# Kernel optimization log

Hardware: AMD Instinct MI355X
Metric: run time of the kernel (lower is better)

Reference implementation:

```python
import jax, jax.numpy as jnp
import numpy as np

B, H_IMG, W_IMG, DIM, HEADS, WS = 8, 56, 56, 768, 12, 14
SEQ = H_IMG * W_IMG
HEAD_DIM = DIM // HEADS
MLP_HID = 4 * DIM
SCALE = HEAD_DIM ** -0.5


def setup_inputs() -> dict:
    key = jax.random.key(0)
    ks = jax.random.split(key, 8)
    s = 0.02
    return {
        "x": jax.random.normal(ks[0], (B, SEQ, DIM), jnp.float32),
        "ln1_scale": jnp.ones((DIM,), jnp.float32),
        "ln1_bias": jnp.zeros((DIM,), jnp.float32),
        "qkv_w": jax.random.normal(ks[1], (DIM, 3 * DIM), jnp.float32) * s,
        "qkv_b": jnp.zeros((3 * DIM,), jnp.float32),
        "rel_pos_h": jax.random.normal(ks[2], (2 * WS - 1, HEAD_DIM), jnp.float32) * s,
        "rel_pos_w": jax.random.normal(ks[3], (2 * WS - 1, HEAD_DIM), jnp.float32) * s,
        "proj_w": jax.random.normal(ks[4], (DIM, DIM), jnp.float32) * s,
        "proj_b": jnp.zeros((DIM,), jnp.float32),
        "ln2_scale": jnp.ones((DIM,), jnp.float32),
        "ln2_bias": jnp.zeros((DIM,), jnp.float32),
        "fc1_w": jax.random.normal(ks[5], (DIM, MLP_HID), jnp.float32) * s,
        "fc1_b": jnp.zeros((MLP_HID,), jnp.float32),
        "fc2_w": jax.random.normal(ks[6], (MLP_HID, DIM), jnp.float32) * s,
        "fc2_b": jnp.zeros((DIM,), jnp.float32),
        "H": H_IMG,
        "W": W_IMG,
    }


def _layernorm(x, scale, bias, eps=1e-5):
    mu = x.mean(-1, keepdims=True)
    var = x.var(-1, keepdims=True)
    return (x - mu) / jnp.sqrt(var + eps) * scale + bias


def _window_attn(x, H, W, qkv_w, qkv_b, rel_pos_h, rel_pos_w, proj_w, proj_b):
    # x: (B, H*W, C); H, W divisible by WS so the torch pad branch is a no-op
    Bn, N, C = x.shape
    nh, nw = H // WS, W // WS
    # window_partition: (B, H, W, C) -> (B*nh*nw, WS*WS, C)
    xw = (x.reshape(Bn, nh, WS, nw, WS, C)
            .transpose(0, 1, 3, 2, 4, 5)
            .reshape(-1, WS * WS, C))
    Bw, Nw = xw.shape[0], WS * WS
    qkv = (xw @ qkv_w + qkv_b).reshape(Bw, Nw, 3, HEADS, HEAD_DIM).transpose(2, 0, 3, 1, 4)
    q = qkv[0] * SCALE  # scaled q also used for rel-pos terms (matches torch)
    k, v = qkv[1], qkv[2]
    attn = jnp.einsum('bhnd,bhmd->bhnm', q, k)  # (Bw, heads, Nw, Nw)
    # relative position bias (q_shape == k_shape == (WS, WS), ratios == 1)
    dist = jnp.arange(WS)[:, None] - jnp.arange(WS)[None, :] + (WS - 1)
    Rh = rel_pos_h[dist]  # (WS, WS, head_dim)
    Rw = rel_pos_w[dist]
    r_q = q.reshape(Bw, HEADS, WS, WS, HEAD_DIM)
    rel_h = jnp.einsum('byhwc,hkc->byhwk', r_q, Rh)
    rel_w = jnp.einsum('byhwc,wkc->byhwk', r_q, Rw)
    attn = (attn.reshape(Bw, HEADS, WS, WS, WS, WS)
            + rel_h[:, :, :, :, :, None]
            + rel_w[:, :, :, :, None, :]).reshape(Bw, HEADS, Nw, Nw)
    attn = jax.nn.softmax(attn, axis=-1)
    out = jnp.einsum('bhnm,bhmd->bhnd', attn, v).transpose(0, 2, 1, 3).reshape(Bw, Nw, C)
    out = out @ proj_w + proj_b
    # window_reverse: (Bw, WS*WS, C) -> (B, H*W, C)
    out = (out.reshape(Bn, nh, nw, WS, WS, C)
              .transpose(0, 1, 3, 2, 4, 5)
              .reshape(Bn, H * W, C))
    return out


def reference(x, ln1_scale, ln1_bias, qkv_w, qkv_b, rel_pos_h, rel_pos_w,
              proj_w, proj_b, ln2_scale, ln2_bias, fc1_w, fc1_b, fc2_w, fc2_b, H, W):
    a = _window_attn(_layernorm(x, ln1_scale, ln1_bias), H, W,
                     qkv_w, qkv_b, rel_pos_h, rel_pos_w, proj_w, proj_b)
    x = x + a
    h = _layernorm(x, ln2_scale, ln2_bias)
    h = jax.nn.gelu(h @ fc1_w + fc1_b, approximate=False)  # torch nn.GELU is exact erf
    x = x + (h @ fc2_w + fc2_b)
    return x
```

## Files before the change

kernel.cpp:

```cpp
#include <hip/hip_runtime.h>
#include <stdint.h>

typedef unsigned short u16;
typedef __bf16 bf16x8 __attribute__((ext_vector_type(8)));
typedef float f32x4 __attribute__((ext_vector_type(4)));
typedef unsigned uint32x4 __attribute__((ext_vector_type(4)));

#define DEVI __device__ __forceinline__

static constexpr int DIM = 768;
static constexpr int SEQL = 3136;
static constexpr int MROWS = 25088;
static constexpr int HEADS = 12;
static constexpr int HD = 64;
static constexpr int NW = 196;
static constexpr float QSCALE = 0.125f;
static constexpr int ATTN_SMEM = 72704;
static constexpr int GEMM_SMEM = 49152;

DEVI float b2f(u16 u) { union { unsigned i; float f; } v; v.i = ((unsigned)u) << 16; return v.f; }
DEVI u16 f2b(float f) { union { float f; unsigned u; } v; v.f = f; return (u16)((v.u + 0x7FFFu + ((v.u >> 16) & 1u)) >> 16); }
DEVI unsigned pack2(float a, float b) { return (unsigned)f2b(a) | ((unsigned)f2b(b) << 16); }
DEVI bf16x8 u4bf(uint4 u) { union { uint4 a; bf16x8 b; } c; c.a = u; return c.b; }

DEVI void gl_lds16(const void* g, void* l) {
  __builtin_amdgcn_global_load_lds((const __attribute__((address_space(1))) void*)g,
                                   (__attribute__((address_space(3))) void*)l, 16, 0, 0);
}

DEVI bf16x8 ldg_b8(const u16* p) {
  union { uint4 u; bf16x8 v; } r;
  const uint2* p2 = (const uint2*)p;
  uint2 lo = p2[0], hi = p2[1];
  r.u.x = lo.x; r.u.y = lo.y; r.u.z = hi.x; r.u.w = hi.y;
  return r.v;
}

__global__ __launch_bounds__(256) void pack_b(const float* __restrict__ in,
                                              u16* __restrict__ out, int K, int N) {
  int f8 = blockIdx.x * 256 + threadIdx.x;
  int l = f8 & 63;
  int rest = f8 >> 6;
  int s = rest & 1, nf = (rest >> 1) & 3, wn2 = (rest >> 3) & 1, kt = rest >> 4;
  int bn = blockIdx.y;
  int n = bn * 128 + wn2 * 64 + nf * 16 + (l & 15);
  int kb = kt * 64 + s * 32 + (l >> 4) * 8;
  size_t obase = (((size_t)bn * (K >> 6) + kt) * 2 + wn2) * 4096 + (nf * 2 + s) * 512 + (size_t)l * 8;
  #pragma unroll
  for (int e = 0; e < 8; ++e)
    out[obase + e] = f2b(in[(size_t)(kb + e) * N + n]);
}

__global__ __launch_bounds__(256) void cvt_rpb(const float* __restrict__ rph,
                                               const float* __restrict__ rpw,
                                               u16* __restrict__ rpb) {
  int i = blockIdx.x * 256 + threadIdx.x;
  int tbl = i >> 11, r = (i >> 6) & 31, c = i & 63;
  float v = (r < 27) ? (tbl ? rpw : rph)[r * 64 + c] : 0.f;
  rpb[i] = f2b(v);
}

template<bool REMAP>
__global__ __launch_bounds__(256) void ln_kernel(const float* __restrict__ xin,
                                                 const float* __restrict__ g,
                                                 const float* __restrict__ bb,
                                                 u16* __restrict__ outw) {
  __shared__ float red[8];
  const int r = blockIdx.x;
  const int tid = threadIdx.x;
  const float* xr = xin + (size_t)r * DIM;
  float v0 = xr[tid], v1 = xr[tid + 256], v2 = xr[tid + 512];
  float s1 = v0 + v1 + v2;
  float s2 = v0 * v0 + v1 * v1 + v2 * v2;
  #pragma unroll
  for (int o = 32; o > 0; o >>= 1) { s1 += __shfl_down(s1, o); s2 += __shfl_down(s2, o); }
  const int l = tid & 63, w = tid >> 6;
  if (l == 0) { red[w] = s1; red[w + 4] = s2; }
  __syncthreads();
  float ts = red[0] + red[1] + red[2] + red[3];
  float tss = red[4] + red[5] + red[6] + red[7];
  float mean = ts * (1.f / 768.f);
  float var = tss * (1.f / 768.f) - mean * mean;
  float rstd = rsqrtf(var + 1e-5f);
  size_t orow;
  if constexpr (REMAP) {
    int b = r / SEQL, s = r % SEQL;
    int h = s / 56, ww = s % 56;
    orow = (size_t)(b * 16 + (h / 14) * 4 + (ww / 14)) * NW + (h % 14) * 14 + (ww % 14);
  } else {
    orow = (size_t)r;
  }
  u16* orp = outw + orow * DIM;
  orp[tid]       = f2b((v0 - mean) * rstd * g[tid]       + bb[tid]);
  orp[tid + 256] = f2b((v1 - mean) * rstd * g[tid + 256] + bb[tid + 256]);
  orp[tid + 512] = f2b((v2 - mean) * rstd * g[tid + 512] + bb[tid + 512]);
}

struct Epi {
  const float* bias;
  const float* x;
  float* outf;
  u16* q; u16* k; u16* v;
  u16* o16;
};

#define MFMA_BF16 __builtin_amdgcn_mfma_f32_16x16x32_bf16

template<int K, int N, int EPI>
__global__ __launch_bounds__(256, 3)
void gemm6_ep(const u16* __restrict__ A, const u16* __restrict__ Bp, Epi ep) {
  extern __shared__ __align__(16) char gsm[];

  constexpr int NBN = N / 128;
  constexpr int NSTC = NBN / 6;
  constexpr int NKT = K / 64;

  const int tid = threadIdx.x;
  const int l = tid & 63, w = tid >> 6;
  const int lr = l & 15, lg = l >> 4;

  const int nwg = gridDim.x;
  const int cpx = nwg >> 3;
  const int wg = (blockIdx.x & 7) * cpx + (blockIdx.x >> 3);
  const int st = wg / 42, r42 = wg - st * 42;
  const int bm = (st / NSTC) * 7 + r42 / 6;
  const int bn = (st - (st / NSTC) * NSTC) * 6 + r42 - (r42 / 6) * 6;
  const int wm = (w >> 1) * 64, wn = (w & 1) * 64;

  const u16* Ab = A + (size_t)bm * 128 * K;
  const u16* Bw = Bp + (((size_t)bn * NKT) * 2 + (w & 1)) * 4096 + (size_t)l * 8;

  int srcoff[4];
  #pragma unroll
  for (int p = 0; p < 4; ++p) {
    int si = p * 256 + tid;
    int row = si >> 3;
    srcoff[p] = row * K + (((si & 7) ^ (row & 7)) << 3);
  }
  #define STG(kt, buf) do {                                                     \
    char* _d = gsm + (buf) * 16384;                                             \
    _Pragma("unroll")                                                           \
    for (int _p = 0; _p < 4; ++_p)                                              \
      gl_lds16(Ab + srcoff[_p] + (size_t)(kt) * 64, _d + _p * 4096 + tid * 16); \
  } while (0)

  const int p0 = lg ^ (lr & 7);
  const int p1 = p0 ^ 4;

  f32x4 zero4 = {0.f, 0.f, 0.f, 0.f};
  f32x4 acc[4][4];
  #pragma unroll
  for (int i = 0; i < 4; ++i)
    #pragma unroll
    for (int j = 0; j < 4; ++j) acc[i][j] = zero4;

  STG(0, 0);
  STG(1, 1);

  for (int t = 0; t < NKT; ++t) {
    if (t + 1 < NKT) asm volatile("s_waitcnt vmcnt(4)" ::: "memory");
    else             asm volatile("s_waitcnt vmcnt(0)" ::: "memory");
    __builtin_amdgcn_s_barrier();

    uint4 braw[4][2];
    const u16* bt = Bw + (size_t)t * 8192;
    #pragma unroll
    for (int nf = 0; nf < 4; ++nf)
      #pragma unroll
      for (int s = 0; s < 2; ++s)
        braw[nf][s] = *(const uint4*)(bt + (nf * 2 + s) * 512);

    if (t + 2 < NKT) STG(t + 2, (t + 2) % 3);

    const u16* cA = (const u16*)(gsm + (t % 3) * 16384);
    bf16x8 af[4][2];
    #pragma unroll
    for (int mf = 0; mf < 4; ++mf) {
      af[mf][0] = *(const bf16x8*)(cA + (wm + mf * 16 + lr) * 64 + p0 * 8);
      af[mf][1] = *(const bf16x8*)(cA + (wm + mf * 16 + lr) * 64 + p1 * 8);
    }
    __builtin_amdgcn_s_setprio(1);
    #pragma unroll
    for (int mf = 0; mf < 4; ++mf)
      #pragma unroll
      for (int nf = 0; nf < 4; ++nf) {
        acc[mf][nf] = MFMA_BF16(af[mf][0], u4bf(braw[nf][0]), acc[mf][nf], 0, 0, 0);
        acc[mf][nf] = MFMA_BF16(af[mf][1], u4bf(braw[nf][1]), acc[mf][nf], 0, 0, 0);
      }
    __builtin_amdgcn_s_setprio(0);
  }
  #undef STG

  __syncthreads();
  float* tp = (float*)(gsm + w * 8448);
  const int ccl = (l & 3) * 16;
  const int cbase = bn * 128 + wn + ccl;
  f32x4 bs[4];
  #pragma unroll
  for (int jj = 0; jj < 4; ++jj) bs[jj] = *(const f32x4*)(ep.bias + cbase + jj * 4);

  #pragma unroll
  for (int q = 0; q < 2; ++q) {
    if (q == 1) { asm volatile("s_waitcnt lgkmcnt(0)" ::: "memory"); __builtin_amdgcn_sched_barrier(0); }
    #pragma unroll
    for (int mf2 = 0; mf2 < 2; ++mf2)
      #pragma unroll
      for (int nf = 0; nf < 4; ++nf)
        #pragma unroll
        for (int e = 0; e < 4; ++e)
          tp[(mf2 * 16 + lg * 4 + e) * 66 + nf * 16 + lr] = acc[q * 2 + mf2][nf][e];
    asm volatile("s_waitcnt lgkmcnt(0)" ::: "memory");
    __builtin_amdgcn_sched_barrier(0);

    #pragma unroll
    for (int pp = 0; pp < 2; ++pp) {
      const int rowl = pp * 16 + (l >> 2);
      const int r = bm * 128 + wm + q * 32 + rowl;
      const int c = cbase;
      f32x4 vv[4];
      #pragma unroll
      for (int jj = 0; jj < 4; ++jj) {
        #pragma unroll
        for (int j2 = 0; j2 < 4; ++j2)
          vv[jj][j2] = tp[rowl * 66 + ccl + jj * 4 + j2];
        vv[jj] += bs[jj];
      }

      if constexpr (EPI == 0) {
        const int which = c / DIM;
        const int hdc = c - which * DIM;
        const int head = hdc >> 6, d0 = hdc & 63;
        const int win = r / NW, pos = r - win * NW;
        const size_t wh = (size_t)win * HEADS + head;
        if (which == 0) {
          uint32x4 o0, o1;
          o0[0] = pack2(vv[0][0] * QSCALE, vv[0][1] * QSCALE);
          o0[1] = pack2(vv[0][2] * QSCALE, vv[0][3] * QSCALE);
          o0[2] = pack2(vv[1][0] * QSCALE, vv[1][1] * QSCALE);
          o0[3] = pack2(vv[1][2] * QSCALE, vv[1][3] * QSCALE);
          o1[0] = pack2(vv[2][0] * QSCALE, vv[2][1] * QSCALE);
          o1[1] = pack2(vv[2][2] * QSCALE, vv[2][3] * QSCALE);
          o1[2] = pack2(vv[3][0] * QSCALE, vv[3][1] * QSCALE);
          o1[3] = pack2(vv[3][2] * QSCALE, vv[3][3] * QSCALE);
          u16* dst = ep.q + (wh * NW + pos) * HD + d0;
          __builtin_nontemporal_store(o0, (uint32x4*)dst);
          __builtin_nontemporal_store(o1, (uint32x4*)(dst + 8));
        } else if (which == 1) {
          uint32x4 o0, o1;
          o0[0] = pack2(vv[0][0], vv[0][1]); o0[1] = pack2(vv[0][2], vv[0][3]);
          o0[2] = pack2(vv[1][0], vv[1][1]); o0[3] = pack2(vv[1][2], vv[1][3]);
          o1[0] = pack2(vv[2][0], vv[2][1]); o1[1] = pack2(vv[2][2], vv[2][3]);
          o1[2] = pack2(vv[3][0], vv[3][1]); o1[3] = pack2(vv[3][2], vv[3][3]);
          u16* dst = ep.k + (wh * NW + pos) * HD + d0;
          __builtin_nontemporal_store(o0, (uint32x4*)dst);
          __builtin_nontemporal_store(o1, (uint32x4*)(dst + 8));
        } else {
          #pragma unroll
          for (int jj = 0; jj < 4; ++jj)
            #pragma unroll
            for (int j2 = 0; j2 < 4; ++j2)
              __builtin_nontemporal_store(f2b(vv[jj][j2]),
                  ep.v + (wh * HD + d0 + jj * 4 + j2) * NW + pos);
        }
      } else if constexpr (EPI == 1) {
        const int win = r / NW, pos = r - win * NW;
        const int b = win >> 4, wi = win & 15;
        const int hh = (wi >> 2) * 14 + pos / 14;
        const int ww2 = (wi & 3) * 14 + pos % 14;
        const size_t orow = (size_t)b * SEQL + hh * 56 + ww2;
        const f32x4* px = (const f32x4*)(ep.x + orow * DIM + c);
        f32x4* po = (f32x4*)(ep.outf + orow * DIM + c);
        #pragma unroll
        for (int jj = 0; jj < 4; ++jj) {
          f32x4 t2 = px[jj] + vv[jj];
          __builtin_nontemporal_store(t2, po + jj);
        }
      } else if constexpr (EPI == 2) {
        float g[16];
        #pragma unroll
        for (int jj = 0; jj < 4; ++jj)
          #pragma unroll
          for (int j2 = 0; j2 < 4; ++j2) {
            float x2 = vv[jj][j2];
            g[jj * 4 + j2] = 0.5f * x2 * (1.f + erff(x2 * 0.70710678118654752f));
          }
        uint32x4 o0, o1;
        o0[0] = pack2(g[0], g[1]);   o0[1] = pack2(g[2], g[3]);
        o0[2] = pack2(g[4], g[5]);   o0[3] = pack2(g[6], g[7]);
        o1[0] = pack2(g[8], g[9]);   o1[1] = pack2(g[10], g[11]);
        o1[2] = pack2(g[12], g[13]); o1[3] = pack2(g[14], g[15]);
        u16* dst = ep.o16 + (size_t)r * N + c;
        __builtin_nontemporal_store(o0, (uint32x4*)dst);
        __builtin_nontemporal_store(o1, (uint32x4*)(dst + 8));
      } else {
        f32x4* po = (f32x4*)(ep.outf + (size_t)r * N + c);
        #pragma unroll
        for (int jj = 0; jj < 4; ++jj) {
          f32x4 t2 = po[jj] + vv[jj];
          __builtin_nontemporal_store(t2, po + jj);
        }
      }
    }
  }
}

__global__ __launch_bounds__(256, 2)
void attn_kernel(const u16* __restrict__ qbuf, const u16* __restrict__ kbuf,
                 const u16* __restrict__ vt, const u16* __restrict__ rpb,
                 u16* __restrict__ abuf) {
  extern __shared__ __align__(16) char smem[];
  u16* sK = (u16*)smem;
  u16* sP = (u16*)(smem + 26624);
  float* sT = (float*)(smem + 56320);

  const int tid = threadIdx.x;
  const int l = tid & 63, w = tid >> 6;
  const int lr = l & 15, lg = l >> 4;
  const int wh = blockIdx.x;
  const int win = wh / HEADS, head = wh - win * HEADS;

  const u16* Qg = qbuf + (size_t)wh * (NW * HD);
  const u16* Kg = kbuf + (size_t)wh * (NW * HD);
  const u16* Vg = vt + (size_t)wh * (HD * NW);

  for (int t = tid; t < 1664; t += 256) {
    int r8 = t >> 3, c8 = t & 7;
    int s = (t & ~7) | (c8 ^ (r8 & 7));
    if (s >= 1568) s &= 1023;
    gl_lds16(Kg + s * 8, (char*)sK + t * 16);
  }
  __syncthreads();

  f32x4 zero4 = {0.f, 0.f, 0.f, 0.f};
  u16* myP = sP + w * (16 * 232);
  float* myT = sT + w * (16 * 64);

  for (int c = 0; c < 4; ++c) {
    const int chunk = w + 4 * c;
    if (chunk > 12) break;

    int qrow = chunk * 16 + lr; if (qrow > 195) qrow = 195;
    bf16x8 aq0 = *(const bf16x8*)(Qg + (size_t)qrow * HD + lg * 8);
    bf16x8 aq1 = *(const bf16x8*)(Qg + (size_t)qrow * HD + 32 + lg * 8);

    f32x4 th[2], tw[2];
    #pragma unroll
    for (int nf2 = 0; nf2 < 2; ++nf2) {
      const u16* bh = rpb + (nf2 * 16 + lr) * 64;
      const u16* bw = rpb + 2048 + (nf2 * 16 + lr) * 64;
      f32x4 a = zero4, b = zero4;
      a = MFMA_BF16(aq0, *(const bf16x8*)(bh + lg * 8), a, 0, 0, 0);
      a = MFMA_BF16(aq1, *(const bf16x8*)(bh + 32 + lg * 8), a, 0, 0, 0);
      b = MFMA_BF16(aq0, *(const bf16x8*)(bw + lg * 8), b, 0, 0, 0);
      b = MFMA_BF16(aq1, *(const bf16x8*)(bw + 32 + lg * 8), b, 0, 0, 0);
      th[nf2] = a; tw[nf2] = b;
    }
    #pragma unroll
    for (int nf2 = 0; nf2 < 2; ++nf2)
      #pragma unroll
      for (int e = 0; e < 4; ++e) {
        myT[(lg * 4 + e) * 64 + nf2 * 16 + lr]      = th[nf2][e];
        myT[(lg * 4 + e) * 64 + 32 + nf2 * 16 + lr] = tw[nf2][e];
      }

    f32x4 accs[13];
    #pragma unroll
    for (int nf = 0; nf < 13; ++nf) {
      int krow = nf * 16 + lr;
      int ksw = (krow & 7) << 3;
      bf16x8 b0 = *(const bf16x8*)(sK + krow * 64 + ((lg * 8) ^ ksw));
      bf16x8 b1 = *(const bf16x8*)(sK + krow * 64 + ((32 + lg * 8) ^ ksw));
      f32x4 cc = zero4;
      cc = MFMA_BF16(aq0, b0, cc, 0, 0, 0);
      cc = MFMA_BF16(aq1, b1, cc, 0, 0, 0);
      accs[nf] = cc;
    }

    int ihv[4], iwv[4];
    #pragma unroll
    for (int e = 0; e < 4; ++e) {
      int gi = chunk * 16 + lg * 4 + e;
      ihv[e] = (gi * 9363) >> 17;
      iwv[e] = gi - ihv[e] * 14;
    }
    float mrow[4] = {-3e38f, -3e38f, -3e38f, -3e38f};
    #pragma unroll
    for (int nf = 0; nf < 13; ++nf) {
      int j = nf * 16 + lr;
      int jh = (j * 9363) >> 17;
      int jw = j - jh * 14;
      #pragma unroll
      for (int e = 0; e < 4; ++e) {
        int ic = lg * 4 + e;
        float s = accs[nf][e]
                + myT[ic * 64 + ((ihv[e] - jh + 13) & 63)]
                + myT[ic * 64 + 32 + (iwv[e] - jw + 13)];
        if (nf == 12 && lr >= 4) s = -1e30f;
        accs[nf][e] = s;
        mrow[e] = fmaxf(mrow[e], s);
      }
    }
    #pragma unroll
    for (int e = 0; e < 4; ++e) {
      float v = mrow[e];
      v = fmaxf(v, __shfl_xor(v, 1)); v = fmaxf(v, __shfl_xor(v, 2));
      v = fmaxf(v, __shfl_xor(v, 4)); v = fmaxf(v, __shfl_xor(v, 8));
      mrow[e] = v;
    }
    float ssum[4] = {0.f, 0.f, 0.f, 0.f};
    #pragma unroll
    for (int nf = 0; nf < 13; ++nf)
      #pragma unroll
      for (int e = 0; e < 4; ++e) {
        float p = __expf(accs[nf][e] - mrow[e]);
        accs[nf][e] = p;
        ssum[e] += p;
      }
    #pragma unroll
    for (int e = 0; e < 4; ++e) {
      float v = ssum[e];
      v += __shfl_xor(v, 1); v += __shfl_xor(v, 2);
      v += __shfl_xor(v, 4); v += __shfl_xor(v, 8);
      ssum[e] = 1.f / v;
    }
    #pragma unroll
    for (int nf = 0; nf < 13; ++nf)
      #pragma unroll
      for (int e = 0; e < 4; ++e)
        myP[(lg * 4 + e) * 232 + nf * 16 + lr] = f2b(accs[nf][e] * ssum[e]);
    #pragma unroll
    for (int e = 0; e < 4; ++e)
      myP[(lg * 4 + e) * 232 + 208 + lr] = 0;

    f32x4 acco[4];
    #pragma unroll
    for (int nf = 0; nf < 4; ++nf) acco[nf] = zero4;
    #pragma unroll
    for (int ks = 0; ks < 7; ++ks) {
      bf16x8 ap = *(const bf16x8*)(myP + lr * 232 + ks * 32 + lg * 8);
      #pragma unroll
      for (int nf = 0; nf < 4; ++nf) {
        bf16x8 bv = ldg_b8(Vg + (size_t)(nf * 16 + lr) * NW + ks * 32 + lg * 8);
        acco[nf] = MFMA_BF16(ap, bv, acco[nf], 0, 0, 0);
      }
    }
    u16* ob = abuf + (size_t)win * NW * DIM + head * HD;
    #pragma unroll
    for (int nf = 0; nf < 4; ++nf)
      #pragma unroll
      for (int e = 0; e < 4; ++e) {
        int row = chunk * 16 + lg * 4 + e;
        if (row < 196) ob[(size_t)row * DIM + nf * 16 + lr] = f2b(acco[nf][e]);
      }
  }
}

extern "C" void kernel_launch(void* const* d_in, const int* in_sizes, int n_in,
                              void* d_out, int out_size, void* d_ws, size_t ws_size,
                              hipStream_t stream) {
  (void)in_sizes; (void)n_in; (void)out_size; (void)ws_size;
  const float* x    = (const float*)d_in[0];
  const float* ln1s = (const float*)d_in[1];
  const float* ln1b = (const float*)d_in[2];
  const float* qkvw = (const float*)d_in[3];
  const float* qkvb = (const float*)d_in[4];
  const float* rph  = (const float*)d_in[5];
  const float* rpw  = (const float*)d_in[6];
  const float* pjw  = (const float*)d_in[7];
  const float* pjb  = (const float*)d_in[8];
  const float* ln2s = (const float*)d_in[9];
  const float* ln2b = (const float*)d_in[10];
  const float* f1w  = (const float*)d_in[11];
  const float* f1b  = (const float*)d_in[12];
  const float* f2w  = (const float*)d_in[13];
  const float* f2b_ = (const float*)d_in[14];
  float* out = (float*)d_out;

  char* ws = (char*)d_ws;
  u16* qkvwT = (u16*)ws;
  u16* projwT = qkvwT + 1769472;
  u16* fc1wT  = qkvwT + 2359296;
  u16* fc2wT  = qkvwT + 4718592;
  u16* xw   = (u16*)(ws + 14155776);
  u16* qbuf = (u16*)(ws + 52690944);
  u16* kbuf = qbuf + 19267584;
  u16* vtb  = kbuf + 19267584;
  u16* h2   = (u16*)(ws + 168296448);
  u16* abuf = xw;
  u16* h1   = xw;
  u16* rpb  = h2;

  (void)hipFuncSetAttribute((const void*)attn_kernel,
                            hipFuncAttributeMaxDynamicSharedMemorySize, ATTN_SMEM);
  (void)hipFuncSetAttribute((const void*)gemm6_ep<768, 2304, 0>,
                            hipFuncAttributeMaxDynamicSharedMemorySize, GEMM_SMEM);
  (void)hipFuncSetAttribute((const void*)gemm6_ep<768, 768, 1>,
                            hipFuncAttributeMaxDynamicSharedMemorySize, GEMM_SMEM);
  (void)hipFuncSetAttribute((const void*)gemm6_ep<768, 3072, 2>,
                            hipFuncAttributeMaxDynamicSharedMemorySize, GEMM_SMEM);
  (void)hipFuncSetAttribute((const void*)gemm6_ep<3072, 768, 3>,
                            hipFuncAttributeMaxDynamicSharedMemorySize, GEMM_SMEM);

  pack_b<<<dim3(768 / 16, 2304 / 128), 256, 0, stream>>>(qkvw, qkvwT, 768, 2304);
  pack_b<<<dim3(768 / 16, 768 / 128),  256, 0, stream>>>(pjw, projwT, 768, 768);
  pack_b<<<dim3(768 / 16, 3072 / 128), 256, 0, stream>>>(f1w, fc1wT, 768, 3072);
  pack_b<<<dim3(3072 / 16, 768 / 128), 256, 0, stream>>>(f2w, fc2wT, 3072, 768);
  cvt_rpb<<<16, 256, 0, stream>>>(rph, rpw, rpb);

  ln_kernel<true><<<MROWS, 256, 0, stream>>>(x, ln1s, ln1b, xw);

  { Epi e{}; e.bias = qkvb; e.q = qbuf; e.k = kbuf; e.v = vtb;
    gemm6_ep<768, 2304, 0><<<196 * 18, 256, GEMM_SMEM, stream>>>(xw, qkvwT, e); }

  attn_kernel<<<1536, 256, ATTN_SMEM, stream>>>(qbuf, kbuf, vtb, rpb, abuf);

  { Epi e{}; e.bias = pjb; e.x = x; e.outf = out;
    gemm6_ep<768, 768, 1><<<196 * 6, 256, GEMM_SMEM, stream>>>(abuf, projwT, e); }

  ln_kernel<false><<<MROWS, 256, 0, stream>>>(out, ln2s, ln2b, h2);

  { Epi e{}; e.bias = f1b; e.o16 = h1;
    gemm6_ep<768, 3072, 2><<<196 * 24, 256, GEMM_SMEM, stream>>>(h2, fc1wT, e); }

  { Epi e{}; e.bias = f2b_; e.outf = out;
    gemm6_ep<3072, 768, 3><<<196 * 6, 256, GEMM_SMEM, stream>>>(h1, fc2wT, e); }
}
```

Measured before the change: 805.8 us.

## Enlarge GEMM tiles to 256x256 with 512-thread workgroups

```diff
diff --git a/kernel.cpp b/kernel.cpp
--- a/kernel.cpp
+++ b/kernel.cpp
@@ -16,7 +16,7 @@
 static constexpr int NW = 196;
 static constexpr float QSCALE = 0.125f;
 static constexpr int ATTN_SMEM = 72704;
-static constexpr int GEMM_SMEM = 49152;
+static constexpr int GEMM_SMEM = 98304;
 
 DEVI float b2f(u16 u) { union { unsigned i; float f; } v; v.i = ((unsigned)u) << 16; return v.f; }
 DEVI u16 f2b(float f) { union { float f; unsigned u; } v; v.f = f; return (u16)((v.u + 0x7FFFu + ((v.u >> 16) & 1u)) >> 16); }
@@ -107,50 +107,51 @@
 #define MFMA_BF16 __builtin_amdgcn_mfma_f32_16x16x32_bf16
 
 template<int K, int N, int EPI>
-__global__ __launch_bounds__(256, 3)
-void gemm6_ep(const u16* __restrict__ A, const u16* __restrict__ Bp, Epi ep) {
+__global__ __launch_bounds__(512, 2)
+void gemm7_ep(const u16* __restrict__ A, const u16* __restrict__ Bp, Epi ep) {
   extern __shared__ __align__(16) char gsm[];
 
-  constexpr int NBN = N / 128;
-  constexpr int NSTC = NBN / 6;
+  constexpr int N2 = N / 256;
+  constexpr int STPC = N2 / 3;
   constexpr int NKT = K / 64;
 
   const int tid = threadIdx.x;
   const int l = tid & 63, w = tid >> 6;
   const int lr = l & 15, lg = l >> 4;
 
-  const int nwg = gridDim.x;
-  const int cpx = nwg >> 3;
-  const int wg = (blockIdx.x & 7) * cpx + (blockIdx.x >> 3);
-  const int st = wg / 42, r42 = wg - st * 42;
-  const int bm = (st / NSTC) * 7 + r42 / 6;
-  const int bn = (st - (st / NSTC) * NSTC) * 6 + r42 - (r42 / 6) * 6;
-  const int wm = (w >> 1) * 64, wn = (w & 1) * 64;
-
-  const u16* Ab = A + (size_t)bm * 128 * K;
-  const u16* Bw = Bp + (((size_t)bn * NKT) * 2 + (w & 1)) * 4096 + (size_t)l * 8;
+  const int nwg = gridDim.x, orig = blockIdx.x;
+  const int q8 = nwg >> 3, r8 = nwg & 7;
+  const int xcd = orig & 7, idx8 = orig >> 3;
+  const int wg = (xcd < r8 ? xcd * (q8 + 1) : r8 * (q8 + 1) + (xcd - r8) * q8) + idx8;
+  const int st = wg / 21, r21 = wg - st * 21;
+  const int bm = (st / STPC) * 7 + r21 / 3;
+  const int bn2 = (st - (st / STPC) * STPC) * 3 + (r21 - (r21 / 3) * 3);
+  const int wm = (w >> 2) * 128, wn = (w & 3) * 64;
+
+  const u16* Ab = A + (size_t)bm * 256 * K;
+  const u16* Bw = Bp + (size_t)(bn2 * 2 + ((w & 3) >> 1)) * NKT * 8192
+                     + (size_t)((w & 3) & 1) * 4096 + (size_t)l * 8;
 
   int srcoff[4];
   #pragma unroll
   for (int p = 0; p < 4; ++p) {
-    int si = p * 256 + tid;
-    int row = si >> 3;
-    srcoff[p] = row * K + (((si & 7) ^ (row & 7)) << 3);
+    int row = p * 64 + (tid >> 3);
+    srcoff[p] = row * K + (((tid & 7) ^ (row & 7)) << 3);
   }
   #define STG(kt, buf) do {                                                     \
-    char* _d = gsm + (buf) * 16384;                                             \
+    char* _d = gsm + (buf) * 32768;                                             \
     _Pragma("unroll")                                                           \
     for (int _p = 0; _p < 4; ++_p)                                              \
-      gl_lds16(Ab + srcoff[_p] + (size_t)(kt) * 64, _d + _p * 4096 + tid * 16); \
+      gl_lds16(Ab + srcoff[_p] + (size_t)(kt) * 64, _d + _p * 8192 + tid * 16); \
   } while (0)
 
   const int p0 = lg ^ (lr & 7);
   const int p1 = p0 ^ 4;
 
   f32x4 zero4 = {0.f, 0.f, 0.f, 0.f};
-  f32x4 acc[4][4];
+  f32x4 acc[8][4];
   #pragma unroll
-  for (int i = 0; i < 4; ++i)
+  for (int i = 0; i < 8; ++i)
     #pragma unroll
     for (int j = 0; j < 4; ++j) acc[i][j] = zero4;
 
@@ -158,8 +159,7 @@
   STG(1, 1);
 
   for (int t = 0; t < NKT; ++t) {
-    if (t + 1 < NKT) asm volatile("s_waitcnt vmcnt(4)" ::: "memory");
-    else             asm volatile("s_waitcnt vmcnt(0)" ::: "memory");
+    if (t == 0) asm volatile("s_waitcnt vmcnt(4)" ::: "memory");
     __builtin_amdgcn_s_barrier();
 
     uint4 braw[4][2];
@@ -172,16 +172,16 @@
 
     if (t + 2 < NKT) STG(t + 2, (t + 2) % 3);
 
-    const u16* cA = (const u16*)(gsm + (t % 3) * 16384);
-    bf16x8 af[4][2];
-    #pragma unroll
-    for (int mf = 0; mf < 4; ++mf) {
+    const u16* cA = (const u16*)(gsm + (t % 3) * 32768);
+    bf16x8 af[8][2];
+    #pragma unroll
+    for (int mf = 0; mf < 8; ++mf) {
       af[mf][0] = *(const bf16x8*)(cA + (wm + mf * 16 + lr) * 64 + p0 * 8);
       af[mf][1] = *(const bf16x8*)(cA + (wm + mf * 16 + lr) * 64 + p1 * 8);
     }
     __builtin_amdgcn_s_setprio(1);
     #pragma unroll
-    for (int mf = 0; mf < 4; ++mf)
+    for (int mf = 0; mf < 8; ++mf)
       #pragma unroll
       for (int nf = 0; nf < 4; ++nf) {
         acc[mf][nf] = MFMA_BF16(af[mf][0], u4bf(braw[nf][0]), acc[mf][nf], 0, 0, 0);
@@ -194,14 +194,14 @@
   __syncthreads();
   float* tp = (float*)(gsm + w * 8448);
   const int ccl = (l & 3) * 16;
-  const int cbase = bn * 128 + wn + ccl;
+  const int cbase = bn2 * 256 + wn + ccl;
   f32x4 bs[4];
   #pragma unroll
   for (int jj = 0; jj < 4; ++jj) bs[jj] = *(const f32x4*)(ep.bias + cbase + jj * 4);
 
   #pragma unroll
-  for (int q = 0; q < 2; ++q) {
-    if (q == 1) { asm volatile("s_waitcnt lgkmcnt(0)" ::: "memory"); __builtin_amdgcn_sched_barrier(0); }
+  for (int q = 0; q < 4; ++q) {
+    if (q) { asm volatile("s_waitcnt lgkmcnt(0)" ::: "memory"); __builtin_amdgcn_sched_barrier(0); }
     #pragma unroll
     for (int mf2 = 0; mf2 < 2; ++mf2)
       #pragma unroll
@@ -215,7 +215,7 @@
     #pragma unroll
     for (int pp = 0; pp < 2; ++pp) {
       const int rowl = pp * 16 + (l >> 2);
-      const int r = bm * 128 + wm + q * 32 + rowl;
+      const int r = bm * 256 + wm + q * 32 + rowl;
       const int c = cbase;
       f32x4 vv[4];
       #pragma unroll
@@ -492,13 +492,13 @@
 
   (void)hipFuncSetAttribute((const void*)attn_kernel,
                             hipFuncAttributeMaxDynamicSharedMemorySize, ATTN_SMEM);
-  (void)hipFuncSetAttribute((const void*)gemm6_ep<768, 2304, 0>,
+  (void)hipFuncSetAttribute((const void*)gemm7_ep<768, 2304, 0>,
                             hipFuncAttributeMaxDynamicSharedMemorySize, GEMM_SMEM);
-  (void)hipFuncSetAttribute((const void*)gemm6_ep<768, 768, 1>,
+  (void)hipFuncSetAttribute((const void*)gemm7_ep<768, 768, 1>,
                             hipFuncAttributeMaxDynamicSharedMemorySize, GEMM_SMEM);
-  (void)hipFuncSetAttribute((const void*)gemm6_ep<768, 3072, 2>,
+  (void)hipFuncSetAttribute((const void*)gemm7_ep<768, 3072, 2>,
                             hipFuncAttributeMaxDynamicSharedMemorySize, GEMM_SMEM);
-  (void)hipFuncSetAttribute((const void*)gemm6_ep<3072, 768, 3>,
+  (void)hipFuncSetAttribute((const void*)gemm7_ep<3072, 768, 3>,
                             hipFuncAttributeMaxDynamicSharedMemorySize, GEMM_SMEM);
 
   pack_b<<<dim3(768 / 16, 2304 / 128), 256, 0, stream>>>(qkvw, qkvwT, 768, 2304);
@@ -510,18 +510,18 @@
   ln_kernel<true><<<MROWS, 256, 0, stream>>>(x, ln1s, ln1b, xw);
 
   { Epi e{}; e.bias = qkvb; e.q = qbuf; e.k = kbuf; e.v = vtb;
-    gemm6_ep<768, 2304, 0><<<196 * 18, 256, GEMM_SMEM, stream>>>(xw, qkvwT, e); }
+    gemm7_ep<768, 2304, 0><<<98 * 9, 512, GEMM_SMEM, stream>>>(xw, qkvwT, e); }
 
   attn_kernel<<<1536, 256, ATTN_SMEM, stream>>>(qbuf, kbuf, vtb, rpb, abuf);
 
   { Epi e{}; e.bias = pjb; e.x = x; e.outf = out;
-    gemm6_ep<768, 768, 1><<<196 * 6, 256, GEMM_SMEM, stream>>>(abuf, projwT, e); }
+    gemm7_ep<768, 768, 1><<<98 * 3, 512, GEMM_SMEM, stream>>>(abuf, projwT, e); }
 
   ln_kernel<false><<<MROWS, 256, 0, stream>>>(out, ln2s, ln2b, h2);
 
   { Epi e{}; e.bias = f1b; e.o16 = h1;
-    gemm6_ep<768, 3072, 2><<<196 * 24, 256, GEMM_SMEM, stream>>>(h2, fc1wT, e); }
+    gemm7_ep<768, 3072, 2><<<98 * 12, 512, GEMM_SMEM, stream>>>(h2, fc1wT, e); }
 
   { Epi e{}; e.bias = f2b_; e.outf = out;
-    gemm6_ep<3072, 768, 3><<<196 * 6, 256, GEMM_SMEM, stream>>>(h1, fc2wT, e); }
-}
+    gemm7_ep<3072, 768, 3><<<98 * 3, 512, GEMM_SMEM, stream>>>(h1, fc2wT, e); }
+}
```

Result: slower. 1.063 ms (+31.9%).
